# Performance work log

Measured on AMD Instinct MI355X. Metric: run time of the kernel, lower is better.

Reference implementation:

```python
import jax, jax.numpy as jnp
import numpy as np


def binarize(w):
    # sign-binarization with straight-through estimator (identity grad)
    return w + jax.lax.stop_gradient(jnp.sign(w) - w)


def setup_inputs() -> dict:
    key = jax.random.key(0)
    ks = jax.random.split(key, 9)
    B, D_IN, H, D_OUT = 524288, 196, 128, 10
    s_in = 1.0 / np.sqrt(D_IN)
    s_h = 1.0 / np.sqrt(H)
    return {
        "x": jax.random.normal(ks[0], (B, D_IN), dtype=jnp.float32),
        "W1": jax.random.uniform(ks[1], (H, D_IN), jnp.float32, -s_in, s_in),
        "b1": jax.random.uniform(ks[2], (H,), jnp.float32, -s_in, s_in),
        "W2": jax.random.uniform(ks[3], (H, H), jnp.float32, -s_h, s_h),
        "b2": jax.random.uniform(ks[4], (H,), jnp.float32, -s_h, s_h),
        "W3": jax.random.uniform(ks[5], (H, H), jnp.float32, -s_h, s_h),
        "b3": jax.random.uniform(ks[6], (H,), jnp.float32, -s_h, s_h),
        "W4": jax.random.uniform(ks[7], (D_OUT, H), jnp.float32, -s_h, s_h),
        "b4": jax.random.uniform(ks[8], (D_OUT,), jnp.float32, -s_h, s_h),
    }


def reference(x, W1, b1, W2, b2, W3, b3, W4, b4):
    # x: [B, 196] (already flat). Hidden layers use binarized weights + ReLU.
    h = jax.nn.relu(x @ binarize(W1).T + b1)   # [B, 128]
    h = jax.nn.relu(h @ binarize(W2).T + b2)   # [B, 128]
    h = jax.nn.relu(h @ binarize(W3).T + b3)   # [B, 128]
    return h @ W4.T + b4                        # [B, 10] (full-precision head)
```

## Files before the change

### kernel.cpp

```cpp
#include <hip/hip_runtime.h>
#include <cstdint>


typedef __attribute__((ext_vector_type(8))) short bf16x8;
typedef __attribute__((ext_vector_type(4))) float f32x4;

typedef unsigned short u16;
typedef unsigned int u32;

#define WS_W1 0
#define WS_W2 28672
#define WS_W3 45056
#define WS_W4 61440
#define WS_TOTAL 63488

__device__ __forceinline__ u32 bf16_rne(float x) {
  u32 u = __float_as_uint(x);
  return (u + 0x7FFFu + ((u >> 16) & 1u)) >> 16;
}

__device__ __forceinline__ u16 sign_bf16(float v) {
  return (v > 0.f) ? 0x3F80u : ((v < 0.f) ? 0xBF80u : 0u);
}

__device__ __forceinline__ int kperm_inv(int p) {
  return ((p & 31) >> 1) + ((p & 1) << 4) + ((p >> 5) << 5);
}

__global__ __launch_bounds__(256) void prep_kernel(
    const float* __restrict__ W1, const float* __restrict__ W2,
    const float* __restrict__ W3, const float* __restrict__ W4,
    u16* __restrict__ ws) {
  int idx = blockIdx.x * 256 + threadIdx.x;
  if (idx < WS_W2) {
    int n = idx / 224, k = idx - n * 224;
    float v = (k < 196) ? W1[n * 196 + k] : 0.f;
    ws[idx] = (k < 196) ? sign_bf16(v) : 0u;
  } else if (idx < WS_W3) {
    int j = idx - WS_W2; int n = j >> 7, p = j & 127;
    ws[idx] = sign_bf16(W2[(n << 7) + kperm_inv(p)]);
  } else if (idx < WS_W4) {
    int j = idx - WS_W3; int n = j >> 7, p = j & 127;
    ws[idx] = sign_bf16(W3[(n << 7) + kperm_inv(p)]);
  } else if (idx < WS_TOTAL) {
    int j = idx - WS_W4; int c = j >> 7, p = j & 127;
    ws[idx] = (c < 10) ? (u16)bf16_rne(W4[(c << 7) + kperm_inv(p)]) : 0u;
  }
}

template <int KP, int SSTR>
__device__ __forceinline__ void layer_fwd(
    const char* __restrict__ src, char* __restrict__ dst,
    const u16* __restrict__ Wp, const float* __restrict__ bias,
    int m, int q, int wr, int wc) {
  f32x4 acc[2][4];
#pragma unroll
  for (int rt = 0; rt < 2; ++rt)
#pragma unroll
    for (int ct = 0; ct < 4; ++ct)
      acc[rt][ct] = (f32x4){0.f, 0.f, 0.f, 0.f};

  const u16* wb = Wp + (wc * 64 + m) * KP + q * 8;
  const char* ab = src + (wr * 32 + m) * SSTR + q * 16;

#pragma unroll
  for (int ks = 0; ks < KP / 32; ++ks) {
    bf16x8 b[4];
#pragma unroll
    for (int ct = 0; ct < 4; ++ct)
      b[ct] = *(const bf16x8*)(wb + ct * 16 * KP + ks * 32);
#pragma unroll
    for (int rt = 0; rt < 2; ++rt) {
      bf16x8 a = *(const bf16x8*)(ab + rt * 16 * SSTR + ks * 64);
#pragma unroll
      for (int ct = 0; ct < 4; ++ct)
        acc[rt][ct] =
            __builtin_amdgcn_mfma_f32_16x16x32_bf16(a, b[ct], acc[rt][ct], 0, 0, 0);
    }
  }

#pragma unroll
  for (int rt = 0; rt < 2; ++rt) {
#pragma unroll
    for (int cp = 0; cp < 2; ++cp) {
      int g = wc * 2 + cp;
      float bi0 = bias[g * 32 + m];
      float bi1 = bias[g * 32 + 16 + m];
#pragma unroll
      for (int j = 0; j < 4; ++j) {
        float v0 = fmaxf(acc[rt][2 * cp][j] + bi0, 0.f);
        float v1 = fmaxf(acc[rt][2 * cp + 1][j] + bi1, 0.f);
        int row = wr * 32 + rt * 16 + q * 4 + j;
        *(u32*)(dst + row * 272 + m * 4 + g * 64) =
            bf16_rne(v0) | (bf16_rne(v1) << 16);
      }
    }
  }
}

__global__ __launch_bounds__(256, 2) void mlp_kernel(
    const float* __restrict__ x, const u16* __restrict__ ws,
    const float* __restrict__ b1, const float* __restrict__ b2,
    const float* __restrict__ b3, const float* __restrict__ b4,
    float* __restrict__ out) {
  __shared__ char smemA[64 * 448];
  __shared__ char smemB[64 * 272];

  const int tid = threadIdx.x;
  const int lane = tid & 63;
  const int wave = tid >> 6;
  const int m = lane & 15;
  const int q = lane >> 4;
  const int wr = wave >> 1, wc = wave & 1;
  const size_t rowbase = (size_t)blockIdx.x * 64;

  const float4* xsrc = (const float4*)(x + rowbase * 196);
#pragma unroll
  for (int it = 0; it < 13; ++it) {
    int i = it * 256 + tid;
    if (i < 3136) {
      float4 v = xsrc[i];
      int r = i / 49;
      int c4 = i - r * 49;
      u32 lo = bf16_rne(v.x) | (bf16_rne(v.y) << 16);
      u32 hi = bf16_rne(v.z) | (bf16_rne(v.w) << 16);
      *(uint2*)(smemA + r * 448 + c4 * 8) = make_uint2(lo, hi);
    }
  }
  for (int i = tid; i < 448; i += 256) {
    int r = i / 7, c = i - r * 7;
    *(uint2*)(smemA + r * 448 + 392 + c * 8) = make_uint2(0u, 0u);
  }
  __syncthreads();

  layer_fwd<224, 448>(smemA, smemB, ws + WS_W1, b1, m, q, wr, wc);
  __syncthreads();
  layer_fwd<128, 272>(smemB, smemA, ws + WS_W2, b2, m, q, wr, wc);
  __syncthreads();
  layer_fwd<128, 272>(smemA, smemB, ws + WS_W3, b3, m, q, wr, wc);
  __syncthreads();

  {
    const int rb = wave * 16;
    f32x4 acc = (f32x4){0.f, 0.f, 0.f, 0.f};
    const char* ab = smemB + (rb + m) * 272 + q * 16;
    const u16* wb = ws + WS_W4 + m * 128 + q * 8;
#pragma unroll
    for (int ks = 0; ks < 4; ++ks) {
      bf16x8 a = *(const bf16x8*)(ab + ks * 64);
      bf16x8 b = *(const bf16x8*)(wb + ks * 32);
      acc = __builtin_amdgcn_mfma_f32_16x16x32_bf16(a, b, acc, 0, 0, 0);
    }
    if (m < 10) {
      float bi = b4[m];
#pragma unroll
      for (int j = 0; j < 4; ++j) {
        size_t row = rowbase + rb + q * 4 + j;
        out[row * 10 + m] = acc[j] + bi;
      }
    }
  }
}

extern "C" void kernel_launch(void* const* d_in, const int* in_sizes, int n_in,
                              void* d_out, int out_size, void* d_ws, size_t ws_size,
                              hipStream_t stream) {
  const float* x  = (const float*)d_in[0];
  const float* W1 = (const float*)d_in[1];
  const float* b1 = (const float*)d_in[2];
  const float* W2 = (const float*)d_in[3];
  const float* b2 = (const float*)d_in[4];
  const float* W3 = (const float*)d_in[5];
  const float* b3 = (const float*)d_in[6];
  const float* W4 = (const float*)d_in[7];
  const float* b4 = (const float*)d_in[8];
  u16* ws = (u16*)d_ws;
  float* out = (float*)d_out;

  prep_kernel<<<248, 256, 0, stream>>>(W1, W2, W3, W4, ws);
  mlp_kernel<<<8192, 256, 0, stream>>>(x, ws, b1, b2, b3, b4, out);
}
```

Measured before the change: 686.5 us.

## Give each wave its own 32-row tile and load x directly into MFMA fragments

Restructures the fused MLP so each wave owns 32 rows and all 128 output columns, keeping activations in a private LDS slice. This removes block-wide __syncthreads between layers. Layer 1 now reads x straight from global memory with nontemporal loads into bf16 MFMA fragments instead of staging it through LDS. Blocks now cover 128 rows, occupancy is raised to 3 blocks per CU, and bf16 packing uses the HIP intrinsic. In exchange, accumulator register pressure doubles (16 f32x4 per wave), and the per-lane global reads of x are strided by row and poorly coalesced.

Result: slower. 776.5 us (+13.1%).

```diff
diff --git a/kernel.cpp b/kernel.cpp
--- a/kernel.cpp
+++ b/kernel.cpp
@@ -1,9 +1,11 @@
 #include <hip/hip_runtime.h>
+#include <hip/hip_bf16.h>
 #include <cstdint>
 
 
 typedef __attribute__((ext_vector_type(8))) short bf16x8;
 typedef __attribute__((ext_vector_type(4))) float f32x4;
+typedef __attribute__((ext_vector_type(4))) float vf4;
 
 typedef unsigned short u16;
 typedef unsigned int u32;
@@ -14,9 +16,16 @@
 #define WS_W4 61440
 #define WS_TOTAL 63488
 
+#define HSTR 272
+
 __device__ __forceinline__ u32 bf16_rne(float x) {
   u32 u = __float_as_uint(x);
   return (u + 0x7FFFu + ((u >> 16) & 1u)) >> 16;
+}
+
+__device__ __forceinline__ u32 pack2(float a, float b) {
+  __hip_bfloat162 p = __float22bfloat162_rn(make_float2(a, b));
+  return *(u32*)&p;
 }
 
 __device__ __forceinline__ u16 sign_bf16(float v) {
@@ -48,115 +57,151 @@
   }
 }
 
-template <int KP, int SSTR>
-__device__ __forceinline__ void layer_fwd(
-    const char* __restrict__ src, char* __restrict__ dst,
-    const u16* __restrict__ Wp, const float* __restrict__ bias,
-    int m, int q, int wr, int wc) {
-  f32x4 acc[2][4];
+__device__ __forceinline__ bf16x8 cvt_frag(vf4 v0, vf4 v1) {
+  union { bf16x8 f; u32 u[4]; } r;
+  r.u[0] = pack2(v0.x, v0.y);
+  r.u[1] = pack2(v0.z, v0.w);
+  r.u[2] = pack2(v1.x, v1.y);
+  r.u[3] = pack2(v1.z, v1.w);
+  return r.f;
+}
+
+__device__ __forceinline__ void epilogue_relu_pack(
+    char* hb, const f32x4 acc[2][8], const float* __restrict__ bias,
+    int m, int q) {
+#pragma unroll
+  for (int rt = 0; rt < 2; ++rt) {
+#pragma unroll
+    for (int g = 0; g < 4; ++g) {
+      float bi0 = bias[g * 32 + m];
+      float bi1 = bias[g * 32 + 16 + m];
+#pragma unroll
+      for (int j = 0; j < 4; ++j) {
+        float v0 = fmaxf(acc[rt][2 * g][j] + bi0, 0.f);
+        float v1 = fmaxf(acc[rt][2 * g + 1][j] + bi1, 0.f);
+        int r = rt * 16 + q * 4 + j;
+        *(u32*)(hb + r * HSTR + g * 64 + m * 4) = pack2(v0, v1);
+      }
+    }
+  }
+}
+
+__device__ __forceinline__ void layer_lds128(
+    char* hb, const u16* __restrict__ Wp, const float* __restrict__ bias,
+    int m, int q) {
+  f32x4 acc[2][8];
 #pragma unroll
   for (int rt = 0; rt < 2; ++rt)
 #pragma unroll
-    for (int ct = 0; ct < 4; ++ct)
+    for (int ct = 0; ct < 8; ++ct)
       acc[rt][ct] = (f32x4){0.f, 0.f, 0.f, 0.f};
 
-  const u16* wb = Wp + (wc * 64 + m) * KP + q * 8;
-  const char* ab = src + (wr * 32 + m) * SSTR + q * 16;
-
-#pragma unroll
-  for (int ks = 0; ks < KP / 32; ++ks) {
-    bf16x8 b[4];
-#pragma unroll
-    for (int ct = 0; ct < 4; ++ct)
-      b[ct] = *(const bf16x8*)(wb + ct * 16 * KP + ks * 32);
+  const char* ab = hb + m * HSTR + q * 16;
+  const u16* wb = Wp + m * 128 + q * 8;
+#pragma unroll
+  for (int ks = 0; ks < 4; ++ks) {
+    bf16x8 b[8];
+#pragma unroll
+    for (int ct = 0; ct < 8; ++ct)
+      b[ct] = *(const bf16x8*)(wb + ct * 2048 + ks * 32);
 #pragma unroll
     for (int rt = 0; rt < 2; ++rt) {
-      bf16x8 a = *(const bf16x8*)(ab + rt * 16 * SSTR + ks * 64);
-#pragma unroll
-      for (int ct = 0; ct < 4; ++ct)
+      bf16x8 a = *(const bf16x8*)(ab + rt * 16 * HSTR + ks * 64);
+#pragma unroll
+      for (int ct = 0; ct < 8; ++ct)
         acc[rt][ct] =
             __builtin_amdgcn_mfma_f32_16x16x32_bf16(a, b[ct], acc[rt][ct], 0, 0, 0);
     }
   }
-
-#pragma unroll
-  for (int rt = 0; rt < 2; ++rt) {
-#pragma unroll
-    for (int cp = 0; cp < 2; ++cp) {
-      int g = wc * 2 + cp;
-      float bi0 = bias[g * 32 + m];
-      float bi1 = bias[g * 32 + 16 + m];
-#pragma unroll
-      for (int j = 0; j < 4; ++j) {
-        float v0 = fmaxf(acc[rt][2 * cp][j] + bi0, 0.f);
-        float v1 = fmaxf(acc[rt][2 * cp + 1][j] + bi1, 0.f);
-        int row = wr * 32 + rt * 16 + q * 4 + j;
-        *(u32*)(dst + row * 272 + m * 4 + g * 64) =
-            bf16_rne(v0) | (bf16_rne(v1) << 16);
-      }
-    }
-  }
-}
-
-__global__ __launch_bounds__(256, 2) void mlp_kernel(
+  epilogue_relu_pack(hb, acc, bias, m, q);
+}
+
+__global__ __launch_bounds__(256, 3) void mlp_kernel(
     const float* __restrict__ x, const u16* __restrict__ ws,
     const float* __restrict__ b1, const float* __restrict__ b2,
     const float* __restrict__ b3, const float* __restrict__ b4,
     float* __restrict__ out) {
-  __shared__ char smemA[64 * 448];
-  __shared__ char smemB[64 * 272];
+  __shared__ char smem[4 * 32 * HSTR];
 
   const int tid = threadIdx.x;
   const int lane = tid & 63;
   const int wave = tid >> 6;
   const int m = lane & 15;
   const int q = lane >> 4;
-  const int wr = wave >> 1, wc = wave & 1;
-  const size_t rowbase = (size_t)blockIdx.x * 64;
-
-  const float4* xsrc = (const float4*)(x + rowbase * 196);
-#pragma unroll
-  for (int it = 0; it < 13; ++it) {
-    int i = it * 256 + tid;
-    if (i < 3136) {
-      float4 v = xsrc[i];
-      int r = i / 49;
-      int c4 = i - r * 49;
-      u32 lo = bf16_rne(v.x) | (bf16_rne(v.y) << 16);
-      u32 hi = bf16_rne(v.z) | (bf16_rne(v.w) << 16);
-      *(uint2*)(smemA + r * 448 + c4 * 8) = make_uint2(lo, hi);
-    }
-  }
-  for (int i = tid; i < 448; i += 256) {
-    int r = i / 7, c = i - r * 7;
-    *(uint2*)(smemA + r * 448 + 392 + c * 8) = make_uint2(0u, 0u);
-  }
-  __syncthreads();
-
-  layer_fwd<224, 448>(smemA, smemB, ws + WS_W1, b1, m, q, wr, wc);
-  __syncthreads();
-  layer_fwd<128, 272>(smemB, smemA, ws + WS_W2, b2, m, q, wr, wc);
-  __syncthreads();
-  layer_fwd<128, 272>(smemA, smemB, ws + WS_W3, b3, m, q, wr, wc);
-  __syncthreads();
+  char* hb = smem + wave * (32 * HSTR);
+  const size_t row0 = (size_t)blockIdx.x * 128 + wave * 32;
 
   {
-    const int rb = wave * 16;
-    f32x4 acc = (f32x4){0.f, 0.f, 0.f, 0.f};
-    const char* ab = smemB + (rb + m) * 272 + q * 16;
+    f32x4 acc[2][8];
+#pragma unroll
+    for (int rt = 0; rt < 2; ++rt)
+#pragma unroll
+      for (int ct = 0; ct < 8; ++ct)
+        acc[rt][ct] = (f32x4){0.f, 0.f, 0.f, 0.f};
+
+    const float* xr0 = x + (row0 + m) * 196;
+    const float* xr1 = xr0 + 16 * 196;
+    const u16* wb = ws + WS_W1 + m * 224 + q * 8;
+
+#pragma unroll
+    for (int ks = 0; ks < 7; ++ks) {
+      bf16x8 b[8];
+#pragma unroll
+      for (int ct = 0; ct < 8; ++ct)
+        b[ct] = *(const bf16x8*)(wb + ct * 3584 + ks * 32);
+
+      bf16x8 a[2];
+      if (ks < 6) {
+        const vf4* p0 = (const vf4*)(xr0 + ks * 32 + q * 8);
+        const vf4* p1 = (const vf4*)(xr1 + ks * 32 + q * 8);
+        vf4 u0 = __builtin_nontemporal_load(p0);
+        vf4 u1 = __builtin_nontemporal_load(p0 + 1);
+        vf4 v0 = __builtin_nontemporal_load(p1);
+        vf4 v1 = __builtin_nontemporal_load(p1 + 1);
+        a[0] = cvt_frag(u0, u1);
+        a[1] = cvt_frag(v0, v1);
+      } else {
+        vf4 z = (vf4){0.f, 0.f, 0.f, 0.f};
+        vf4 u0 = z, v0 = z;
+        if (q == 0) {
+          u0 = __builtin_nontemporal_load((const vf4*)(xr0 + 192));
+          v0 = __builtin_nontemporal_load((const vf4*)(xr1 + 192));
+        }
+        a[0] = cvt_frag(u0, z);
+        a[1] = cvt_frag(v0, z);
+      }
+#pragma unroll
+      for (int rt = 0; rt < 2; ++rt)
+#pragma unroll
+        for (int ct = 0; ct < 8; ++ct)
+          acc[rt][ct] =
+              __builtin_amdgcn_mfma_f32_16x16x32_bf16(a[rt], b[ct], acc[rt][ct], 0, 0, 0);
+    }
+    epilogue_relu_pack(hb, acc, b1, m, q);
+  }
+
+  layer_lds128(hb, ws + WS_W2, b2, m, q);
+  layer_lds128(hb, ws + WS_W3, b3, m, q);
+
+  {
     const u16* wb = ws + WS_W4 + m * 128 + q * 8;
-#pragma unroll
-    for (int ks = 0; ks < 4; ++ks) {
-      bf16x8 a = *(const bf16x8*)(ab + ks * 64);
-      bf16x8 b = *(const bf16x8*)(wb + ks * 32);
-      acc = __builtin_amdgcn_mfma_f32_16x16x32_bf16(a, b, acc, 0, 0, 0);
-    }
-    if (m < 10) {
-      float bi = b4[m];
-#pragma unroll
-      for (int j = 0; j < 4; ++j) {
-        size_t row = rowbase + rb + q * 4 + j;
-        out[row * 10 + m] = acc[j] + bi;
+    const char* ab = hb + m * HSTR + q * 16;
+#pragma unroll
+    for (int rt = 0; rt < 2; ++rt) {
+      f32x4 acc = (f32x4){0.f, 0.f, 0.f, 0.f};
+#pragma unroll
+      for (int ks = 0; ks < 4; ++ks) {
+        bf16x8 a = *(const bf16x8*)(ab + rt * 16 * HSTR + ks * 64);
+        bf16x8 b = *(const bf16x8*)(wb + ks * 32);
+        acc = __builtin_amdgcn_mfma_f32_16x16x32_bf16(a, b, acc, 0, 0, 0);
+      }
+      if (m < 10) {
+        float bi = b4[m];
+#pragma unroll
+        for (int j = 0; j < 4; ++j) {
+          size_t r = row0 + rt * 16 + q * 4 + j;
+          out[r * 10 + m] = acc[j] + bi;
+        }
       }
     }
   }
@@ -178,5 +223,5 @@
   float* out = (float*)d_out;
 
   prep_kernel<<<248, 256, 0, stream>>>(W1, W2, W3, W4, ws);
-  mlp_kernel<<<8192, 256, 0, stream>>>(x, ws, b1, b2, b3, b4, out);
-}
+  mlp_kernel<<<4096, 256, 0, stream>>>(x, ws, b1, b2, b3, b4, out);
+}
```
